# Kernel tuning notes

Measured on AMD Instinct MI355X. Metric: run time of the kernel, lower is better.

## Reference

```python
import jax, jax.numpy as jnp
import numpy as np

N = 20000      # nodes
E = 320000     # edges
D = 128        # h feature dim
L = 2          # EGCL layers
MH = 256       # mlp_m hidden
MO = 128       # mlp_m output (message dim)
XH = 256       # mlp_x hidden
HH = 256       # mlp_h hidden
MIN = 2 * D + 1  # 257: cat(h_i, h_j, ||dx||^2)


def silu(z):
    return z * jax.nn.sigmoid(z)


def setup_inputs() -> dict:
    key = jax.random.key(0)
    ks = jax.random.split(key, 18)
    s = 0.05
    return {
        "edge_index": jax.random.randint(ks[0], (2, E), 0, N, dtype=jnp.int64 if jax.config.jax_enable_x64 else jnp.int32),
        "h": jax.random.normal(ks[1], (N, D), dtype=jnp.float32),
        "x": jax.random.normal(ks[2], (N, 3), dtype=jnp.float32),
        # per-layer stacked MLP params
        "Wm1": jax.random.normal(ks[3], (L, MIN, MH), dtype=jnp.float32) * s,
        "bm1": jnp.zeros((L, MH), dtype=jnp.float32),
        "Wm2": jax.random.normal(ks[4], (L, MH, MO), dtype=jnp.float32) * s,
        "bm2": jnp.zeros((L, MO), dtype=jnp.float32),
        "Wx1": jax.random.normal(ks[5], (L, MIN, XH), dtype=jnp.float32) * s,
        "bx1": jnp.zeros((L, XH), dtype=jnp.float32),
        "Wx2": jax.random.normal(ks[6], (L, XH, 3), dtype=jnp.float32) * s,
        "bx2": jnp.zeros((L, 3), dtype=jnp.float32),
        "Wh1": jax.random.normal(ks[7], (L, D + MO, HH), dtype=jnp.float32) * s,
        "bh1": jnp.zeros((L, HH), dtype=jnp.float32),
        "Wh2": jax.random.normal(ks[8], (L, HH, D), dtype=jnp.float32) * s,
        "bh2": jnp.zeros((L, D), dtype=jnp.float32),
        "Wa": jax.random.normal(ks[9], (L, MO, 1), dtype=jnp.float32) * s,
        "ba": jnp.zeros((L, 1), dtype=jnp.float32),
    }


def reference(edge_index, h, x, Wm1, bm1, Wm2, bm2, Wx1, bx1, Wx2, bx2,
              Wh1, bh1, Wh2, bh2, Wa, ba):
    # flow='target_to_source': i = edge_index[0], j = edge_index[1],
    # aggregation (scatter-sum) indexed by edge_index[0].
    src = edge_index[0]
    dst = edge_index[1]
    n_nodes = h.shape[0]
    n_layers = Wm1.shape[0]
    for l in range(n_layers):
        hi, hj = h[src], h[dst]                       # [E, D] gathers
        diff = x[src] - x[dst]                        # [E, 3]
        d2 = jnp.sum(diff * diff, axis=1, keepdims=True)  # ||dx||^2, [E, 1]
        feat = jnp.concatenate([hi, hj, d2], axis=1)  # [E, 2D+1]
        # --- h message: mlp_m + sigmoid attention gate ---
        m = silu(feat @ Wm1[l] + bm1[l]) @ Wm2[l] + bm2[l]   # [E, MO]
        m = m * jax.nn.sigmoid(m @ Wa[l] + ba[l])
        agg_h = jax.ops.segment_sum(m, src, num_segments=n_nodes)  # [N, MO]
        new_h = silu(jnp.concatenate([h, agg_h], axis=1) @ Wh1[l] + bh1[l]) @ Wh2[l] + bh2[l]
        # --- x message (uses OLD h, as in original forward) ---
        mx = silu(feat @ Wx1[l] + bx1[l]) @ Wx2[l] + bx2[l]  # [E, 3]
        # NOTE: original uses torch.norm(coords_i - coords_j) with NO dim ->
        # a single global Frobenius norm over all edges; reproduced faithfully.
        gnorm = jnp.sqrt(jnp.sum(diff * diff))
        xm = diff * mx / (gnorm + 1.0)                # [E, 3]
        new_x = x + jax.ops.segment_sum(xm, src, num_segments=n_nodes)
        h, x = new_h, new_x
    return (h, x)
```

## Files before the change

kernel.cpp:

```cpp
#include <hip/hip_runtime.h>
#include <hip/hip_bf16.h>

#define N_NODES 20000
#define N_EDGES 320000
#define D 128

typedef __attribute__((ext_vector_type(8))) short short8;
typedef __attribute__((ext_vector_type(4))) float f32x4;

__device__ __forceinline__ float sigmoid_f(float z) { return 1.f / (1.f + __expf(-z)); }
__device__ __forceinline__ float silu_f(float z) { return z * sigmoid_f(z); }
__device__ __forceinline__ short f2bf(float f) {
    union { float f; unsigned u; } a; a.f = f;
    unsigned r = a.u + 0x7fff + ((a.u >> 16) & 1);
    return (short)(r >> 16);
}
__device__ __forceinline__ float bf2f(short s) {
    union { unsigned u; float f; } a; a.u = ((unsigned)(unsigned short)s) << 16;
    return a.f;
}

__global__ void precompute_kernel(const int* __restrict__ ei,
                                  const float* __restrict__ x,
                                  float* __restrict__ gsum) {
    int e = blockIdx.x * blockDim.x + threadIdx.x;
    float local = 0.f;
    if (e < N_EDGES) {
        int s = ei[e];
        int d = ei[N_EDGES + e];
        float dx = x[s * 3 + 0] - x[d * 3 + 0];
        float dy = x[s * 3 + 1] - x[d * 3 + 1];
        float dz = x[s * 3 + 2] - x[d * 3 + 2];
        local = dx * dx + dy * dy + dz * dz;
    }
    #pragma unroll
    for (int o = 32; o > 0; o >>= 1) local += __shfl_down(local, o, 64);
    if ((threadIdx.x & 63) == 0) atomicAdd(gsum, local);
}

__global__ void prep_weights(const float* __restrict__ Wm1, const float* __restrict__ Wx1,
                             const float* __restrict__ Wm2, const float* __restrict__ Wh1,
                             const float* __restrict__ Wh2,
                             short* __restrict__ WcatT, short* __restrict__ Wm2T,
                             short* __restrict__ Wh1T, short* __restrict__ Wh2T) {
    int idx = blockIdx.x * 256 + threadIdx.x;
    if (idx < 131072) {
        int seg = idx >> 15, r = idx & 32767, k = r >> 8, c = r & 255;
        const float* s = (seg == 0) ? Wm1 : (seg == 1) ? Wm1 + 128 * 256
                        : (seg == 2) ? Wx1 : Wx1 + 128 * 256;
        WcatT[(size_t)(seg * 256 + c) * 128 + k] = f2bf(s[k * 256 + c]);
    } else if (idx < 163840) {
        int r = idx - 131072, k = r >> 7, c = r & 127;
        Wm2T[c * 256 + k] = f2bf(Wm2[k * 128 + c]);
    } else if (idx < 229376) {
        int r = idx - 163840, k = r >> 8, c = r & 255;
        Wh1T[c * 256 + k] = f2bf(Wh1[k * 256 + c]);
    } else {
        int r = idx - 229376, k = r >> 7, c = r & 127;
        Wh2T[c * 256 + k] = f2bf(Wh2[k * 128 + c]);
    }
}

__global__ __launch_bounds__(256, 4) void tgemm_kernel(const float* __restrict__ h,
        const short* __restrict__ WcatT, short* __restrict__ T) {
    int tid = threadIdx.x, w = tid >> 6, l = tid & 63;
    int l15 = l & 15, kg = l >> 4;
    int rowbase = blockIdx.x * 64 + w * 16;
    int cg = blockIdx.y;
    int arow = rowbase + l15; if (arow >= N_NODES) arow = N_NODES - 1;
    f32x4 acc[16];
    #pragma unroll
    for (int ct = 0; ct < 16; ct++) acc[ct] = (f32x4){0.f, 0.f, 0.f, 0.f};
    #pragma unroll
    for (int ks = 0; ks < 4; ks++) {
        int kb = ks * 32 + kg * 8;
        const f32x4* hp = (const f32x4*)(h + (size_t)arow * 128 + kb);
        f32x4 h0 = hp[0], h1 = hp[1];
        short8 a;
        a[0] = f2bf(h0.x); a[1] = f2bf(h0.y); a[2] = f2bf(h0.z); a[3] = f2bf(h0.w);
        a[4] = f2bf(h1.x); a[5] = f2bf(h1.y); a[6] = f2bf(h1.z); a[7] = f2bf(h1.w);
        #pragma unroll
        for (int ct = 0; ct < 16; ct++) {
            short8 b = *(const short8*)(WcatT + (size_t)(cg * 256 + ct * 16 + l15) * 128 + kb);
            acc[ct] = __builtin_amdgcn_mfma_f32_16x16x32_bf16(a, b, acc[ct], 0, 0, 0);
        }
    }
    #pragma unroll
    for (int ct = 0; ct < 16; ct++) {
        #pragma unroll
        for (int r = 0; r < 4; r++) {
            int node = rowbase + kg * 4 + r;
            if (node < N_NODES)
                T[(size_t)node * 1024 + cg * 256 + ct * 16 + l15] = f2bf(acc[ct][r]);
        }
    }
}

__global__ __launch_bounds__(256, 4) void edge_kernel(
    const int* __restrict__ ei, const short* __restrict__ T,
    const float* __restrict__ xc, const float* __restrict__ gsum,
    const float* __restrict__ Wm1r, const float* __restrict__ bm1,
    const short* __restrict__ Wm2T, const float* __restrict__ bm2,
    const float* __restrict__ Wa, const float* __restrict__ ba,
    const float* __restrict__ Wx1r, const float* __restrict__ bx1,
    const float* __restrict__ Wx2, const float* __restrict__ bx2,
    float* __restrict__ agg_h, float* __restrict__ aggx) {
    int tid = threadIdx.x, w = tid >> 6, l = tid & 63;
    int l15 = l & 15, kg = l >> 4;
    int ebase = blockIdx.x * 64 + w * 16;
    int e = ebase + l15;
    int src = ei[e], dst = ei[N_EDGES + e];
    float dfx = xc[src * 3 + 0] - xc[dst * 3 + 0];
    float dfy = xc[src * 3 + 1] - xc[dst * 3 + 1];
    float dfz = xc[src * 3 + 2] - xc[dst * 3 + 2];
    float d2v = dfx * dfx + dfy * dfy + dfz * dfz;

    f32x4 acc[8];
    #pragma unroll
    for (int ct = 0; ct < 8; ct++) { float bv = bm2[ct * 16 + l15]; acc[ct] = (f32x4){bv, bv, bv, bv}; }
    #pragma unroll
    for (int ks = 0; ks < 8; ks++) {
        int cb = ks * 32 + kg * 8;
        short8 ts = *(const short8*)(T + (size_t)src * 1024 + cb);
        short8 td = *(const short8*)(T + (size_t)dst * 1024 + 256 + cb);
        f32x4 w0 = ((const f32x4*)(Wm1r + cb))[0], w1 = ((const f32x4*)(Wm1r + cb))[1];
        f32x4 b0 = ((const f32x4*)(bm1 + cb))[0], b1 = ((const f32x4*)(bm1 + cb))[1];
        float wv[8], bv[8];
        *(f32x4*)&wv[0] = w0; *(f32x4*)&wv[4] = w1;
        *(f32x4*)&bv[0] = b0; *(f32x4*)&bv[4] = b1;
        short8 a;
        #pragma unroll
        for (int i = 0; i < 8; i++) {
            float z = bf2f(ts[i]) + bf2f(td[i]) + d2v * wv[i] + bv[i];
            a[i] = f2bf(silu_f(z));
        }
        #pragma unroll
        for (int ct = 0; ct < 8; ct++) {
            short8 b = *(const short8*)(Wm2T + (size_t)(ct * 16 + l15) * 256 + cb);
            acc[ct] = __builtin_amdgcn_mfma_f32_16x16x32_bf16(a, b, acc[ct], 0, 0, 0);
        }
    }
    float part[4] = {0.f, 0.f, 0.f, 0.f};
    #pragma unroll
    for (int ct = 0; ct < 8; ct++) {
        float wa = Wa[ct * 16 + l15];
        #pragma unroll
        for (int r = 0; r < 4; r++) part[r] += acc[ct][r] * wa;
    }
    #pragma unroll
    for (int m = 1; m < 16; m <<= 1) {
        #pragma unroll
        for (int r = 0; r < 4; r++) part[r] += __shfl_xor(part[r], m, 64);
    }
    float ba0 = ba[0];
    float gate[4];
    int srow[4];
    #pragma unroll
    for (int r = 0; r < 4; r++) {
        gate[r] = sigmoid_f(part[r] + ba0);
        srow[r] = ei[ebase + kg * 4 + r];
    }
    #pragma unroll
    for (int ct = 0; ct < 8; ct++)
        #pragma unroll
        for (int r = 0; r < 4; r++)
            atomicAdd(&agg_h[(size_t)srow[r] * 128 + ct * 16 + l15], acc[ct][r] * gate[r]);

    float px[3] = {0.f, 0.f, 0.f};
    #pragma unroll
    for (int ks = 0; ks < 8; ks++) {
        int cb = ks * 32 + kg * 8;
        short8 ts = *(const short8*)(T + (size_t)src * 1024 + 512 + cb);
        short8 td = *(const short8*)(T + (size_t)dst * 1024 + 768 + cb);
        f32x4 w0 = ((const f32x4*)(Wx1r + cb))[0], w1 = ((const f32x4*)(Wx1r + cb))[1];
        f32x4 b0 = ((const f32x4*)(bx1 + cb))[0], b1 = ((const f32x4*)(bx1 + cb))[1];
        float wv[8], bv[8];
        *(f32x4*)&wv[0] = w0; *(f32x4*)&wv[4] = w1;
        *(f32x4*)&bv[0] = b0; *(f32x4*)&bv[4] = b1;
        float wx[24];
        const f32x4* xp = (const f32x4*)(Wx2 + cb * 3);
        #pragma unroll
        for (int q = 0; q < 6; q++) *(f32x4*)&wx[q * 4] = xp[q];
        #pragma unroll
        for (int i = 0; i < 8; i++) {
            float z = silu_f(bf2f(ts[i]) + bf2f(td[i]) + d2v * wv[i] + bv[i]);
            px[0] += z * wx[i * 3 + 0];
            px[1] += z * wx[i * 3 + 1];
            px[2] += z * wx[i * 3 + 2];
        }
    }
    #pragma unroll
    for (int m = 16; m < 64; m <<= 1) {
        #pragma unroll
        for (int c = 0; c < 3; c++) px[c] += __shfl_xor(px[c], m, 64);
    }
    if (kg == 0) {
        float gn = sqrtf(gsum[0]);
        float invg = 1.f / (gn + 1.f);
        float df[3] = {dfx, dfy, dfz};
        #pragma unroll
        for (int c = 0; c < 3; c++) {
            float mx = px[c] + bx2[c];
            float xm = df[c] * mx * invg;
            atomicAdd(&aggx[(size_t)src * 3 + c], xm);
        }
    }
}

__global__ __launch_bounds__(256, 4) void node_kernel(
    const float* __restrict__ hc, const float* __restrict__ xc,
    const float* __restrict__ agg_h, const float* __restrict__ aggx,
    const short* __restrict__ Wh1T, const float* __restrict__ bh1,
    const short* __restrict__ Wh2T, const float* __restrict__ bh2,
    float* __restrict__ ho, float* __restrict__ xo) {
    __shared__ short sH[64][264];
    int tid = threadIdx.x, w = tid >> 6, l = tid & 63;
    int l15 = l & 15, kg = l >> 4;
    int nbase = blockIdx.x * 64;
    int arow = nbase + w * 16 + l15;
    int arc = (arow < N_NODES) ? arow : (N_NODES - 1);

    f32x4 acc1[16];
    #pragma unroll
    for (int ct = 0; ct < 16; ct++) { float bv = bh1[ct * 16 + l15]; acc1[ct] = (f32x4){bv, bv, bv, bv}; }
    #pragma unroll
    for (int ks = 0; ks < 8; ks++) {
        int kb = ks * 32 + kg * 8;
        const float* sp = (kb < 128) ? (hc + (size_t)arc * 128 + kb)
                                     : (agg_h + (size_t)arc * 128 + (kb - 128));
        f32x4 h0 = ((const f32x4*)sp)[0], h1 = ((const f32x4*)sp)[1];
        short8 a;
        a[0] = f2bf(h0.x); a[1] = f2bf(h0.y); a[2] = f2bf(h0.z); a[3] = f2bf(h0.w);
        a[4] = f2bf(h1.x); a[5] = f2bf(h1.y); a[6] = f2bf(h1.z); a[7] = f2bf(h1.w);
        #pragma unroll
        for (int ct = 0; ct < 16; ct++) {
            short8 b = *(const short8*)(Wh1T + (size_t)(ct * 16 + l15) * 256 + kb);
            acc1[ct] = __builtin_amdgcn_mfma_f32_16x16x32_bf16(a, b, acc1[ct], 0, 0, 0);
        }
    }
    #pragma unroll
    for (int ct = 0; ct < 16; ct++)
        #pragma unroll
        for (int r = 0; r < 4; r++)
            sH[w * 16 + kg * 4 + r][ct * 16 + l15] = f2bf(silu_f(acc1[ct][r]));
    __syncthreads();

    f32x4 acc2[8];
    #pragma unroll
    for (int ct = 0; ct < 8; ct++) { float bv = bh2[ct * 16 + l15]; acc2[ct] = (f32x4){bv, bv, bv, bv}; }
    #pragma unroll
    for (int ks = 0; ks < 8; ks++) {
        int kb = ks * 32 + kg * 8;
        short8 a = *(const short8*)&sH[w * 16 + l15][kb];
        #pragma unroll
        for (int ct = 0; ct < 8; ct++) {
            short8 b = *(const short8*)(Wh2T + (size_t)(ct * 16 + l15) * 256 + kb);
            acc2[ct] = __builtin_amdgcn_mfma_f32_16x16x32_bf16(a, b, acc2[ct], 0, 0, 0);
        }
    }
    #pragma unroll
    for (int ct = 0; ct < 8; ct++)
        #pragma unroll
        for (int r = 0; r < 4; r++) {
            int node = nbase + w * 16 + kg * 4 + r;
            if (node < N_NODES) ho[(size_t)node * 128 + ct * 16 + l15] = acc2[ct][r];
        }

    if (tid < 192) {
        int nn = tid / 3, c = tid - nn * 3;
        int node = nbase + nn;
        if (node < N_NODES)
            xo[(size_t)node * 3 + c] = xc[(size_t)node * 3 + c] + aggx[(size_t)node * 3 + c];
    }
}

extern "C" void kernel_launch(void* const* d_in, const int* in_sizes, int n_in,
                              void* d_out, int out_size, void* d_ws, size_t ws_size,
                              hipStream_t stream) {
    const int* ei = (const int*)d_in[0];
    const float* h_in = (const float*)d_in[1];
    const float* x_in = (const float*)d_in[2];
    const float* Wm1 = (const float*)d_in[3];
    const float* bm1 = (const float*)d_in[4];
    const float* Wm2 = (const float*)d_in[5];
    const float* bm2 = (const float*)d_in[6];
    const float* Wx1 = (const float*)d_in[7];
    const float* bx1 = (const float*)d_in[8];
    const float* Wx2 = (const float*)d_in[9];
    const float* bx2 = (const float*)d_in[10];
    const float* Wh1 = (const float*)d_in[11];
    const float* bh1 = (const float*)d_in[12];
    const float* Wh2 = (const float*)d_in[13];
    const float* bh2 = (const float*)d_in[14];
    const float* Wa = (const float*)d_in[15];
    const float* ba = (const float*)d_in[16];

    char* wsb = (char*)d_ws;
    short* T     = (short*)wsb;                 wsb += (size_t)N_NODES * 1024 * 2;
    short* WcatT = (short*)wsb;                 wsb += (size_t)1024 * 128 * 2;
    short* Wm2T  = (short*)wsb;                 wsb += (size_t)128 * 256 * 2;
    short* Wh1T  = (short*)wsb;                 wsb += (size_t)256 * 256 * 2;
    short* Wh2T  = (short*)wsb;                 wsb += (size_t)128 * 256 * 2;
    float* agg_h = (float*)wsb;                 wsb += (size_t)N_NODES * 128 * 4;
    float* aggx  = (float*)wsb;                 wsb += (size_t)N_NODES * 3 * 4;
    float* gsum  = (float*)wsb;                 wsb += 16;

    float* h_out_f = (float*)d_out;
    float* x_out_f = h_out_f + (size_t)N_NODES * D;

    for (int l = 0; l < 2; l++) {
        const float* hc = (l == 0) ? h_in : h_out_f;
        const float* xc = (l == 0) ? x_in : x_out_f;
        float* ho = h_out_f;
        float* xo = x_out_f;

        const float* Wm1_l = Wm1 + (size_t)l * 257 * 256;
        const float* Wx1_l = Wx1 + (size_t)l * 257 * 256;

        hipMemsetAsync(gsum, 0, sizeof(float), stream);
        hipMemsetAsync(agg_h, 0, sizeof(float) * (size_t)N_NODES * 128, stream);
        hipMemsetAsync(aggx, 0, sizeof(float) * (size_t)N_NODES * 3, stream);

        prep_weights<<<1024, 256, 0, stream>>>(
            Wm1_l, Wx1_l, Wm2 + (size_t)l * 256 * 128,
            Wh1 + (size_t)l * 256 * 256, Wh2 + (size_t)l * 256 * 128,
            WcatT, Wm2T, Wh1T, Wh2T);

        precompute_kernel<<<(N_EDGES + 255) / 256, 256, 0, stream>>>(ei, xc, gsum);

        tgemm_kernel<<<dim3((N_NODES + 63) / 64, 4), 256, 0, stream>>>(hc, WcatT, T);

        edge_kernel<<<N_EDGES / 64, 256, 0, stream>>>(
            ei, T, xc, gsum,
            Wm1_l + 256 * 256, bm1 + (size_t)l * 256,
            Wm2T, bm2 + (size_t)l * 128,
            Wa + (size_t)l * 128, ba + l,
            Wx1_l + 256 * 256, bx1 + (size_t)l * 256,
            Wx2 + (size_t)l * 256 * 3, bx2 + (size_t)l * 3,
            agg_h, aggx);

        node_kernel<<<(N_NODES + 63) / 64, 256, 0, stream>>>(
            hc, xc, agg_h, aggx,
            Wh1T, bh1 + (size_t)l * 256,
            Wh2T, bh2 + (size_t)l * 128,
            ho, xo);
    }
}
```

Baseline: 1.133 ms.

## Sort edges by source, coalesce scatter atomics, and use MFMA for x-message

Adds a counting sort (histogram, scan, scatter) that groups edges by source node once per call, so each edge tile's atomics to agg_h can be merged across consecutive rows that share a source. The T column layout is reordered so the src-side halves of both MLPs sit next to each other, which should improve locality of the per-src gathers. The Wx2 projection becomes an MFMA against a zero-padded transposed weight instead of scalar FMAs plus shuffles. Occupancy launch bounds are raised. In exchange the sort adds several kernels, including a single-block serial scan, and extra shared-memory synchronisation in the edge kernel.

```diff
diff --git a/kernel.cpp b/kernel.cpp
--- a/kernel.cpp
+++ b/kernel.cpp
@@ -20,14 +20,48 @@
     return a.f;
 }
 
-__global__ void precompute_kernel(const int* __restrict__ ei,
+__global__ void hist_kernel(const int* __restrict__ ei, int* __restrict__ hist) {
+    int e = blockIdx.x * 256 + threadIdx.x;
+    if (e < N_EDGES) atomicAdd(&hist[ei[e]], 1);
+}
+
+__global__ void scan_kernel(const int* __restrict__ hist, int* __restrict__ offs) {
+    __shared__ int part[1024];
+    __shared__ int ppre[1024];
+    int t = threadIdx.x;
+    int base = t * 20;
+    int s = 0;
+    for (int j = 0; j < 20; j++) { int i = base + j; if (i < N_NODES) s += hist[i]; }
+    part[t] = s;
+    __syncthreads();
+    if (t == 0) { int acc = 0; for (int i = 0; i < 1024; i++) { ppre[i] = acc; acc += part[i]; } }
+    __syncthreads();
+    int run = ppre[t];
+    for (int j = 0; j < 20; j++) {
+        int i = base + j;
+        if (i < N_NODES) { offs[i] = run; run += hist[i]; }
+    }
+}
+
+__global__ void scatter_kernel(const int* __restrict__ ei, const int* __restrict__ offs,
+                               int* __restrict__ cursor,
+                               int* __restrict__ es, int* __restrict__ ed) {
+    int e = blockIdx.x * 256 + threadIdx.x;
+    if (e < N_EDGES) {
+        int s = ei[e], d = ei[N_EDGES + e];
+        int p = offs[s] + atomicAdd(&cursor[s], 1);
+        es[p] = s; ed[p] = d;
+    }
+}
+
+__global__ void precompute_kernel(const int* __restrict__ es, const int* __restrict__ ed,
                                   const float* __restrict__ x,
                                   float* __restrict__ gsum) {
     int e = blockIdx.x * blockDim.x + threadIdx.x;
     float local = 0.f;
     if (e < N_EDGES) {
-        int s = ei[e];
-        int d = ei[N_EDGES + e];
+        int s = es[e];
+        int d = ed[e];
         float dx = x[s * 3 + 0] - x[d * 3 + 0];
         float dy = x[s * 3 + 1] - x[d * 3 + 1];
         float dz = x[s * 3 + 2] - x[d * 3 + 2];
@@ -40,14 +74,15 @@
 
 __global__ void prep_weights(const float* __restrict__ Wm1, const float* __restrict__ Wx1,
                              const float* __restrict__ Wm2, const float* __restrict__ Wh1,
-                             const float* __restrict__ Wh2,
+                             const float* __restrict__ Wh2, const float* __restrict__ Wx2,
                              short* __restrict__ WcatT, short* __restrict__ Wm2T,
-                             short* __restrict__ Wh1T, short* __restrict__ Wh2T) {
+                             short* __restrict__ Wh1T, short* __restrict__ Wh2T,
+                             short* __restrict__ Wx2T) {
     int idx = blockIdx.x * 256 + threadIdx.x;
     if (idx < 131072) {
         int seg = idx >> 15, r = idx & 32767, k = r >> 8, c = r & 255;
-        const float* s = (seg == 0) ? Wm1 : (seg == 1) ? Wm1 + 128 * 256
-                        : (seg == 2) ? Wx1 : Wx1 + 128 * 256;
+        const float* s = (seg == 0) ? Wm1 : (seg == 1) ? Wx1
+                        : (seg == 2) ? Wm1 + 128 * 256 : Wx1 + 128 * 256;
         WcatT[(size_t)(seg * 256 + c) * 128 + k] = f2bf(s[k * 256 + c]);
     } else if (idx < 163840) {
         int r = idx - 131072, k = r >> 7, c = r & 127;
@@ -55,9 +90,12 @@
     } else if (idx < 229376) {
         int r = idx - 163840, k = r >> 8, c = r & 255;
         Wh1T[c * 256 + k] = f2bf(Wh1[k * 256 + c]);
-    } else {
+    } else if (idx < 262144) {
         int r = idx - 229376, k = r >> 7, c = r & 127;
         Wh2T[c * 256 + k] = f2bf(Wh2[k * 128 + c]);
+    } else {
+        int r = idx - 262144, c = r >> 8, k = r & 255;
+        Wx2T[c * 256 + k] = (c < 3) ? f2bf(Wx2[k * 3 + c]) : (short)0;
     }
 }
 
@@ -96,24 +134,36 @@
     }
 }
 
-__global__ __launch_bounds__(256, 4) void edge_kernel(
-    const int* __restrict__ ei, const short* __restrict__ T,
-    const float* __restrict__ xc, const float* __restrict__ gsum,
+__global__ __launch_bounds__(256, 6) void edge_kernel(
+    const int* __restrict__ es, const int* __restrict__ ed,
+    const short* __restrict__ T, const float* __restrict__ xc,
+    const float* __restrict__ gsum,
     const float* __restrict__ Wm1r, const float* __restrict__ bm1,
     const short* __restrict__ Wm2T, const float* __restrict__ bm2,
     const float* __restrict__ Wa, const float* __restrict__ ba,
     const float* __restrict__ Wx1r, const float* __restrict__ bx1,
-    const float* __restrict__ Wx2, const float* __restrict__ bx2,
+    const short* __restrict__ Wx2T, const float* __restrict__ bx2,
     float* __restrict__ agg_h, float* __restrict__ aggx) {
+    __shared__ float sdiff[64][4];
     int tid = threadIdx.x, w = tid >> 6, l = tid & 63;
     int l15 = l & 15, kg = l >> 4;
     int ebase = blockIdx.x * 64 + w * 16;
     int e = ebase + l15;
-    int src = ei[e], dst = ei[N_EDGES + e];
+    int src = es[e], dst = ed[e];
     float dfx = xc[src * 3 + 0] - xc[dst * 3 + 0];
     float dfy = xc[src * 3 + 1] - xc[dst * 3 + 1];
     float dfz = xc[src * 3 + 2] - xc[dst * 3 + 2];
     float d2v = dfx * dfx + dfy * dfy + dfz * dfz;
+    if (kg == 0) {
+        sdiff[w * 16 + l15][0] = dfx;
+        sdiff[w * 16 + l15][1] = dfy;
+        sdiff[w * 16 + l15][2] = dfz;
+    }
+    __syncthreads();
+
+    int srow[4];
+    #pragma unroll
+    for (int r = 0; r < 4; r++) srow[r] = es[ebase + kg * 4 + r];
 
     f32x4 acc[8];
     #pragma unroll
@@ -122,7 +172,7 @@
     for (int ks = 0; ks < 8; ks++) {
         int cb = ks * 32 + kg * 8;
         short8 ts = *(const short8*)(T + (size_t)src * 1024 + cb);
-        short8 td = *(const short8*)(T + (size_t)dst * 1024 + 256 + cb);
+        short8 td = *(const short8*)(T + (size_t)dst * 1024 + 512 + cb);
         f32x4 w0 = ((const f32x4*)(Wm1r + cb))[0], w1 = ((const f32x4*)(Wm1r + cb))[1];
         f32x4 b0 = ((const f32x4*)(bm1 + cb))[0], b1 = ((const f32x4*)(bm1 + cb))[1];
         float wv[8], bv[8];
@@ -154,55 +204,53 @@
     }
     float ba0 = ba[0];
     float gate[4];
-    int srow[4];
-    #pragma unroll
-    for (int r = 0; r < 4; r++) {
-        gate[r] = sigmoid_f(part[r] + ba0);
-        srow[r] = ei[ebase + kg * 4 + r];
-    }
-    #pragma unroll
-    for (int ct = 0; ct < 8; ct++)
-        #pragma unroll
-        for (int r = 0; r < 4; r++)
-            atomicAdd(&agg_h[(size_t)srow[r] * 128 + ct * 16 + l15], acc[ct][r] * gate[r]);
-
-    float px[3] = {0.f, 0.f, 0.f};
+    #pragma unroll
+    for (int r = 0; r < 4; r++) gate[r] = sigmoid_f(part[r] + ba0);
+    #pragma unroll
+    for (int ct = 0; ct < 8; ct++) {
+        int c = ct * 16 + l15;
+        float run = acc[ct][0] * gate[0];
+        #pragma unroll
+        for (int r = 1; r < 4; r++) {
+            float v = acc[ct][r] * gate[r];
+            if (srow[r] == srow[r - 1]) {
+                run += v;
+            } else {
+                atomicAdd(&agg_h[(size_t)srow[r - 1] * 128 + c], run);
+                run = v;
+            }
+        }
+        atomicAdd(&agg_h[(size_t)srow[3] * 128 + c], run);
+    }
+
+    float bxi = (l15 < 3) ? bx2[l15] : 0.f;
+    f32x4 accx = (f32x4){bxi, bxi, bxi, bxi};
     #pragma unroll
     for (int ks = 0; ks < 8; ks++) {
         int cb = ks * 32 + kg * 8;
-        short8 ts = *(const short8*)(T + (size_t)src * 1024 + 512 + cb);
+        short8 ts = *(const short8*)(T + (size_t)src * 1024 + 256 + cb);
         short8 td = *(const short8*)(T + (size_t)dst * 1024 + 768 + cb);
         f32x4 w0 = ((const f32x4*)(Wx1r + cb))[0], w1 = ((const f32x4*)(Wx1r + cb))[1];
         f32x4 b0 = ((const f32x4*)(bx1 + cb))[0], b1 = ((const f32x4*)(bx1 + cb))[1];
         float wv[8], bv[8];
         *(f32x4*)&wv[0] = w0; *(f32x4*)&wv[4] = w1;
         *(f32x4*)&bv[0] = b0; *(f32x4*)&bv[4] = b1;
-        float wx[24];
-        const f32x4* xp = (const f32x4*)(Wx2 + cb * 3);
-        #pragma unroll
-        for (int q = 0; q < 6; q++) *(f32x4*)&wx[q * 4] = xp[q];
+        short8 a;
         #pragma unroll
         for (int i = 0; i < 8; i++) {
-            float z = silu_f(bf2f(ts[i]) + bf2f(td[i]) + d2v * wv[i] + bv[i]);
-            px[0] += z * wx[i * 3 + 0];
-            px[1] += z * wx[i * 3 + 1];
-            px[2] += z * wx[i * 3 + 2];
-        }
-    }
-    #pragma unroll
-    for (int m = 16; m < 64; m <<= 1) {
-        #pragma unroll
-        for (int c = 0; c < 3; c++) px[c] += __shfl_xor(px[c], m, 64);
-    }
-    if (kg == 0) {
+            float z = bf2f(ts[i]) + bf2f(td[i]) + d2v * wv[i] + bv[i];
+            a[i] = f2bf(silu_f(z));
+        }
+        short8 b = *(const short8*)(Wx2T + (size_t)l15 * 256 + cb);
+        accx = __builtin_amdgcn_mfma_f32_16x16x32_bf16(a, b, accx, 0, 0, 0);
+    }
+    if (l15 < 3) {
         float gn = sqrtf(gsum[0]);
         float invg = 1.f / (gn + 1.f);
-        float df[3] = {dfx, dfy, dfz};
-        #pragma unroll
-        for (int c = 0; c < 3; c++) {
-            float mx = px[c] + bx2[c];
-            float xm = df[c] * mx * invg;
-            atomicAdd(&aggx[(size_t)src * 3 + c], xm);
+        #pragma unroll
+        for (int r = 0; r < 4; r++) {
+            float df = sdiff[w * 16 + kg * 4 + r][l15];
+            atomicAdd(&aggx[(size_t)srow[r] * 3 + l15], df * accx[r] * invg);
         }
     }
 }
@@ -296,17 +344,29 @@
     const float* ba = (const float*)d_in[16];
 
     char* wsb = (char*)d_ws;
-    short* T     = (short*)wsb;                 wsb += (size_t)N_NODES * 1024 * 2;
-    short* WcatT = (short*)wsb;                 wsb += (size_t)1024 * 128 * 2;
-    short* Wm2T  = (short*)wsb;                 wsb += (size_t)128 * 256 * 2;
-    short* Wh1T  = (short*)wsb;                 wsb += (size_t)256 * 256 * 2;
-    short* Wh2T  = (short*)wsb;                 wsb += (size_t)128 * 256 * 2;
-    float* agg_h = (float*)wsb;                 wsb += (size_t)N_NODES * 128 * 4;
-    float* aggx  = (float*)wsb;                 wsb += (size_t)N_NODES * 3 * 4;
-    float* gsum  = (float*)wsb;                 wsb += 16;
+    short* T      = (short*)wsb;  wsb += (size_t)N_NODES * 1024 * 2;
+    short* WcatT  = (short*)wsb;  wsb += (size_t)1024 * 128 * 2;
+    short* Wm2T   = (short*)wsb;  wsb += (size_t)128 * 256 * 2;
+    short* Wh1T   = (short*)wsb;  wsb += (size_t)256 * 256 * 2;
+    short* Wh2T   = (short*)wsb;  wsb += (size_t)128 * 256 * 2;
+    short* Wx2T   = (short*)wsb;  wsb += (size_t)16 * 256 * 2;
+    float* agg_h  = (float*)wsb;  wsb += (size_t)N_NODES * 128 * 4;
+    float* aggx   = (float*)wsb;  wsb += (size_t)N_NODES * 3 * 4;
+    int*   es     = (int*)wsb;    wsb += (size_t)N_EDGES * 4;
+    int*   ed     = (int*)wsb;    wsb += (size_t)N_EDGES * 4;
+    int*   hist   = (int*)wsb;    wsb += (size_t)N_NODES * 4;
+    int*   cursor = (int*)wsb;    wsb += (size_t)N_NODES * 4;
+    float* gsum   = (float*)wsb;  wsb += 16;
+    int*   offs   = (int*)wsb;    wsb += (size_t)(N_NODES + 16) * 4;
 
     float* h_out_f = (float*)d_out;
     float* x_out_f = h_out_f + (size_t)N_NODES * D;
+
+    hipMemsetAsync(hist, 0, sizeof(int) * N_NODES, stream);
+    hipMemsetAsync(cursor, 0, sizeof(int) * N_NODES, stream);
+    hist_kernel<<<(N_EDGES + 255) / 256, 256, 0, stream>>>(ei, hist);
+    scan_kernel<<<1, 1024, 0, stream>>>(hist, offs);
+    scatter_kernel<<<(N_EDGES + 255) / 256, 256, 0, stream>>>(ei, offs, cursor, es, ed);
 
     for (int l = 0; l < 2; l++) {
         const float* hc = (l == 0) ? h_in : h_out_f;
@@ -321,22 +381,23 @@
         hipMemsetAsync(agg_h, 0, sizeof(float) * (size_t)N_NODES * 128, stream);
         hipMemsetAsync(aggx, 0, sizeof(float) * (size_t)N_NODES * 3, stream);
 
-        prep_weights<<<1024, 256, 0, stream>>>(
+        prep_weights<<<1040, 256, 0, stream>>>(
             Wm1_l, Wx1_l, Wm2 + (size_t)l * 256 * 128,
             Wh1 + (size_t)l * 256 * 256, Wh2 + (size_t)l * 256 * 128,
-            WcatT, Wm2T, Wh1T, Wh2T);
-
-        precompute_kernel<<<(N_EDGES + 255) / 256, 256, 0, stream>>>(ei, xc, gsum);
+            Wx2 + (size_t)l * 256 * 3,
+            WcatT, Wm2T, Wh1T, Wh2T, Wx2T);
+
+        precompute_kernel<<<(N_EDGES + 255) / 256, 256, 0, stream>>>(es, ed, xc, gsum);
 
         tgemm_kernel<<<dim3((N_NODES + 63) / 64, 4), 256, 0, stream>>>(hc, WcatT, T);
 
         edge_kernel<<<N_EDGES / 64, 256, 0, stream>>>(
-            ei, T, xc, gsum,
+            es, ed, T, xc, gsum,
             Wm1_l + 256 * 256, bm1 + (size_t)l * 256,
             Wm2T, bm2 + (size_t)l * 128,
             Wa + (size_t)l * 128, ba + l,
             Wx1_l + 256 * 256, bx1 + (size_t)l * 256,
-            Wx2 + (size_t)l * 256 * 3, bx2 + (size_t)l * 3,
+            Wx2T, bx2 + (size_t)l * 3,
             agg_h, aggx);
 
         node_kernel<<<(N_NODES + 63) / 64, 256, 0, stream>>>(
```

Result: no change. 1.155 ms (+1.9%).
